# Performance work log

Measured on AMD Instinct MI355X. Metric: run time of the kernel, lower is better.

## Reference

```python
import jax, jax.numpy as jnp
import numpy as np

B, N, C, H, W = 4, 262144, 40, 256, 256
HID = 128


def _bilinear_sample(plane, u, v):
    """torch F.grid_sample(mode='bilinear', padding_mode='zeros', align_corners=False).
    plane: (B, C, H, W); u, v: (B, N) in [-1, 1] (u -> width axis, v -> height axis).
    Returns (B, N, C)."""
    Wd, Hd = plane.shape[3], plane.shape[2]
    ix = ((u + 1.0) * Wd - 1.0) * 0.5
    iy = ((v + 1.0) * Hd - 1.0) * 0.5
    ix0 = jnp.floor(ix)
    iy0 = jnp.floor(iy)
    fx = ix - ix0
    fy = iy - iy0
    ix0 = ix0.astype(jnp.int32)
    iy0 = iy0.astype(jnp.int32)
    flat = plane.reshape(plane.shape[0], plane.shape[1], Hd * Wd)  # (B,C,H*W)

    def corner(xi, yi, w):
        valid = (xi >= 0) & (xi < Wd) & (yi >= 0) & (yi < Hd)
        xc = jnp.clip(xi, 0, Wd - 1)
        yc = jnp.clip(yi, 0, Hd - 1)
        idx = yc * Wd + xc  # (B,N)
        vals = jnp.take_along_axis(flat, idx[:, None, :], axis=2)  # (B,C,N)
        return vals * (w * valid)[:, None, :]

    out = (corner(ix0, iy0, (1 - fx) * (1 - fy))
           + corner(ix0 + 1, iy0, fx * (1 - fy))
           + corner(ix0, iy0 + 1, (1 - fx) * fy)
           + corner(ix0 + 1, iy0 + 1, fx * fy))  # (B,C,N)
    return jnp.transpose(out, (0, 2, 1))  # (B,N,C)


def _sample_triplane(triplane, coords):
    x, y, z = coords[..., 0], coords[..., 1], coords[..., 2]
    f_xy = _bilinear_sample(triplane[:, 0], x, y)
    f_xz = _bilinear_sample(triplane[:, 1], x, z)
    f_yz = _bilinear_sample(triplane[:, 2], y, z)
    return jnp.concatenate([f_xy, f_xz, f_yz], axis=-1)  # (B,N,3C)


def setup_inputs() -> dict:
    key = jax.random.key(0)
    ks = jax.random.split(key, 16)
    triplane = jax.random.normal(ks[0], (B, 3, C, H, W), dtype=jnp.float32)
    coords = jax.random.uniform(ks[1], (B, N, 3), dtype=jnp.float32) * 2.0 - 1.0
    vd = jax.random.normal(ks[2], (B, N, 3), dtype=jnp.float32)
    view_dirs = vd / (jnp.linalg.norm(vd, axis=-1, keepdims=True) + 1e-8)
    s = 0.05
    p = {
        'triplane': triplane, 'coords': coords, 'view_dirs': view_dirs,
        'dw1': jax.random.normal(ks[3], (3 * C, HID), dtype=jnp.float32) * s,
        'db1': jnp.zeros((HID,), jnp.float32),
        'dw2': jax.random.normal(ks[4], (HID, HID), dtype=jnp.float32) * s,
        'db2': jnp.zeros((HID,), jnp.float32),
        'dw3': jax.random.normal(ks[5], (HID, 1), dtype=jnp.float32) * s,
        'db3': jnp.zeros((1,), jnp.float32),
        'cw1': jax.random.normal(ks[6], (3 * C + 3, HID), dtype=jnp.float32) * s,
        'cb1': jnp.zeros((HID,), jnp.float32),
        'cw2': jax.random.normal(ks[7], (HID, HID), dtype=jnp.float32) * s,
        'cb2': jnp.zeros((HID,), jnp.float32),
        'cw3': jax.random.normal(ks[8], (HID, 3), dtype=jnp.float32) * s,
        'cb3': jnp.zeros((3,), jnp.float32),
    }
    return p


def reference(triplane, coords, view_dirs, dw1, db1, dw2, db2, dw3, db3,
              cw1, cb1, cw2, cb2, cw3, cb3):
    feats = _sample_triplane(triplane, coords)  # (B,N,3C)
    h = jax.nn.relu(feats @ dw1 + db1)
    h = jax.nn.relu(h @ dw2 + db2)
    density = h @ dw3 + db3  # (B,N,1)
    cin = jnp.concatenate([feats, view_dirs], axis=-1)
    g = jax.nn.relu(cin @ cw1 + cb1)
    g = jax.nn.relu(g @ cw2 + cb2)
    rgb = jax.nn.sigmoid(g @ cw3 + cb3)  # (B,N,3)
    return density, rgb
```

## Files before the change

### kernel.cpp

```cpp
#include <hip/hip_runtime.h>
#include <cstdint>
#include <cstddef>

typedef __bf16 bf16x8 __attribute__((ext_vector_type(8)));
typedef float  f32x4  __attribute__((ext_vector_type(4)));

#define MFMA16(a,b,c) __builtin_amdgcn_mfma_f32_16x16x32_bf16((a),(b),(c),0,0,0)

__device__ __forceinline__ uint f2bf1(float f){
  uint u = __builtin_bit_cast(uint, f);
  u += 0x7FFFu + ((u >> 16) & 1u);
  return u >> 16;
}
__device__ __forceinline__ uint pack2(float a, float b){
  return f2bf1(a) | (f2bf1(b) << 16);
}
__device__ __forceinline__ uint pack2f(float a, float b){
  uint ua = __builtin_bit_cast(uint, a) + 0x8000u;
  uint ub = __builtin_bit_cast(uint, b) + 0x8000u;
  return __builtin_amdgcn_perm(ub, ua, 0x07060302u);
}
__device__ __forceinline__ float bflo(uint d){ return __builtin_bit_cast(float, d << 16); }
__device__ __forceinline__ float bfhi(uint d){ return __builtin_bit_cast(float, d & 0xFFFF0000u); }

__global__ __launch_bounds__(256, 4) void transpose_k(
    const float* __restrict__ tri, ushort* __restrict__ tp)
{
  __shared__ ushort st[64 * 41];
  const int bi  = blockIdx.x;
  const int xb  = bi & 3;
  const int y   = (bi >> 2) & 255;
  const int q   = bi >> 10;
  const int tid = threadIdx.x;
  const float* src = tri + (size_t)q * 40 * 65536 + y * 256 + xb * 64;
#pragma unroll
  for (int it = 0; it < 10; it++){
    int lin = it * 256 + tid;
    int c = lin >> 6, x = lin & 63;
    float v = src[(size_t)c * 65536 + x];
    st[x * 41 + c] = (ushort)f2bf1(v);
  }
  __syncthreads();
  uint* dst = (uint*)(tp + ((size_t)q * 65536 + (size_t)y * 256 + xb * 64) * 40);
#pragma unroll
  for (int it = 0; it < 5; it++){
    int lin = it * 256 + tid;
    int e  = lin * 2;
    int x1 = (e * 1639) >> 16;       int c1 = e  - x1 * 40;
    int e2 = e + 1;
    int x2 = (e2 * 1639) >> 16;      int c2 = e2 - x2 * 40;
    dst[lin] = (uint)st[x1 * 41 + c1] | ((uint)st[x2 * 41 + c2] << 16);
  }
}

__global__ void pack_k(const float* __restrict__ dw1, const float* __restrict__ cw1,
                       const float* __restrict__ dw2, const float* __restrict__ cw2,
                       const float* __restrict__ dw3, const float* __restrict__ cw3,
                       uint4* __restrict__ wpk)
{
  int idx = blockIdx.x * 256 + threadIdx.x;
  if (idx >= 8704) return;
  int mode, rel;
  if      (idx < 2048){ mode = 0; rel = idx; }
  else if (idx < 4096){ mode = 1; rel = idx - 2048; }
  else if (idx < 6144){ mode = 2; rel = idx - 4096; }
  else if (idx < 8192){ mode = 3; rel = idx - 6144; }
  else if (idx < 8448){ mode = 4; rel = idx - 8192; }
  else                { mode = 5; rel = idx - 8448; }
  int frag = rel >> 6, lane = rel & 63;
  int Mt = frag >> 2, s = frag & 3;
  int m  = Mt * 16 + (lane & 15);
  int kb = s * 32 + (lane >> 4) * 8;
  uint d[4];
#pragma unroll
  for (int jj = 0; jj < 4; jj++){
    float v0 = 0.f, v1 = 0.f;
#pragma unroll
    for (int h = 0; h < 2; h++){
      int k = kb + jj * 2 + h;
      float v = 0.f;
      switch (mode){
        case 0: v = (k < 120) ? dw1[k * 128 + m] : 0.f; break;
        case 1: v = (k < 123) ? cw1[k * 128 + m] : 0.f; break;
        case 2: v = dw2[k * 128 + m]; break;
        case 3: v = cw2[k * 128 + m]; break;
        case 4: v = (m == 0) ? dw3[k] : 0.f; break;
        default: v = (m >= 1 && m <= 3) ? cw3[k * 3 + (m - 1)] : 0.f; break;
      }
      if (h == 0) v0 = v; else v1 = v;
    }
    d[jj] = pack2(v0, v1);
  }
  uint4 o; o.x = d[0]; o.y = d[1]; o.z = d[2]; o.w = d[3];
  wpk[idx] = o;
}

__device__ __forceinline__ uint4 blend4(uint4 a, uint4 b, uint4 c, uint4 d,
                                        float w00, float w10, float w01, float w11){
  uint4 ov;
  ov.x = pack2f(w00*bflo(a.x)+w10*bflo(b.x)+w01*bflo(c.x)+w11*bflo(d.x),
                w00*bfhi(a.x)+w10*bfhi(b.x)+w01*bfhi(c.x)+w11*bfhi(d.x));
  ov.y = pack2f(w00*bflo(a.y)+w10*bflo(b.y)+w01*bflo(c.y)+w11*bflo(d.y),
                w00*bfhi(a.y)+w10*bfhi(b.y)+w01*bfhi(c.y)+w11*bfhi(d.y));
  ov.z = pack2f(w00*bflo(a.z)+w10*bflo(b.z)+w01*bflo(c.z)+w11*bflo(d.z),
                w00*bfhi(a.z)+w10*bfhi(b.z)+w01*bfhi(c.z)+w11*bfhi(d.z));
  ov.w = pack2f(w00*bflo(a.w)+w10*bflo(b.w)+w01*bflo(c.w)+w11*bflo(d.w),
                w00*bfhi(a.w)+w10*bfhi(b.w)+w01*bfhi(c.w)+w11*bfhi(d.w));
  return ov;
}

__device__ __forceinline__ bf16x8 read_h(const uint* S, int s, int t, int lrow, int lq){
  int dwb = (s * 16 + lq * 4 + (lrow << 2)) & 63;
  return __builtin_bit_cast(bf16x8, *(const uint4*)&S[(t * 16 + lrow) * 64 + dwb]);
}

__device__ __forceinline__ void put_h(uint* S, f32x4 v, int Mt, int t, int lrow, int lq){
  uint2 w;
  w.x = pack2f(fmaxf(v[0], 0.f), fmaxf(v[1], 0.f));
  w.y = pack2f(fmaxf(v[2], 0.f), fmaxf(v[3], 0.f));
  int dw = (Mt * 8 + lq * 2 + (lrow << 2)) & 63;
  *(uint2*)&S[(t * 16 + lrow) * 64 + dw] = w;
}

__device__ __forceinline__ void layer1(uint* S, const uint4* __restrict__ W,
                                       const float* __restrict__ bias,
                                       const uint4 (&bf)[4][2],
                                       int lrow, int lq, int lane){
  f32x4 acc[8][2];
#pragma unroll
  for (int Mt = 0; Mt < 8; Mt++){
    f32x4 bi = *(const f32x4*)(bias + Mt * 16 + lq * 4);
    acc[Mt][0] = bi; acc[Mt][1] = bi;
  }
#pragma unroll
  for (int s = 0; s < 4; s++)
#pragma unroll
    for (int Mt = 0; Mt < 8; Mt++){
      bf16x8 aw = __builtin_bit_cast(bf16x8, W[(Mt * 4 + s) * 64 + lane]);
      acc[Mt][0] = MFMA16(aw, __builtin_bit_cast(bf16x8, bf[s][0]), acc[Mt][0]);
      acc[Mt][1] = MFMA16(aw, __builtin_bit_cast(bf16x8, bf[s][1]), acc[Mt][1]);
    }
#pragma unroll
  for (int Mt = 0; Mt < 8; Mt++){
    put_h(S, acc[Mt][0], Mt, 0, lrow, lq);
    put_h(S, acc[Mt][1], Mt, 1, lrow, lq);
  }
}

__device__ __forceinline__ void dense_l(uint* S, const uint4* __restrict__ W,
                                        const float* __restrict__ bias,
                                        int lrow, int lq, int lane){
  f32x4 acc[8][2];
#pragma unroll
  for (int Mt = 0; Mt < 8; Mt++){
    f32x4 bi = *(const f32x4*)(bias + Mt * 16 + lq * 4);
    acc[Mt][0] = bi; acc[Mt][1] = bi;
  }
#pragma unroll
  for (int s = 0; s < 4; s++){
    bf16x8 bh0 = read_h(S, s, 0, lrow, lq);
    bf16x8 bh1 = read_h(S, s, 1, lrow, lq);
#pragma unroll
    for (int Mt = 0; Mt < 8; Mt++){
      bf16x8 aw = __builtin_bit_cast(bf16x8, W[(Mt * 4 + s) * 64 + lane]);
      acc[Mt][0] = MFMA16(aw, bh0, acc[Mt][0]);
      acc[Mt][1] = MFMA16(aw, bh1, acc[Mt][1]);
    }
  }
#pragma unroll
  for (int Mt = 0; Mt < 8; Mt++){
    put_h(S, acc[Mt][0], Mt, 0, lrow, lq);
    put_h(S, acc[Mt][1], Mt, 1, lrow, lq);
  }
}

__device__ __forceinline__ void out_l(const uint* S, const uint4* __restrict__ W,
                                      f32x4 (&acc3)[2], int lrow, int lq, int lane){
#pragma unroll
  for (int s = 0; s < 4; s++){
    bf16x8 aw = __builtin_bit_cast(bf16x8, W[s * 64 + lane]);
    acc3[0] = MFMA16(aw, read_h(S, s, 0, lrow, lq), acc3[0]);
    acc3[1] = MFMA16(aw, read_h(S, s, 1, lrow, lq), acc3[1]);
  }
}

__global__ __launch_bounds__(256, 3) void fused_k(
    const ushort* __restrict__ tp, const float* __restrict__ coords,
    const float* __restrict__ vdirs, const uint4* __restrict__ wpk,
    const float* __restrict__ db1, const float* __restrict__ db2,
    const float* __restrict__ db3, const float* __restrict__ cb1,
    const float* __restrict__ cb2, const float* __restrict__ cb3,
    float* __restrict__ out)
{
  __shared__ uint4 sS4[2048];
  const int wave = threadIdx.x >> 6;
  uint* S = (uint*)sS4 + wave * 2048;
  const int lane = threadIdx.x & 63, lrow = lane & 15, lq = lane >> 4;
  const int blk   = blockIdx.x;
  const int pbase = (blk & 3) * 262144 + (blk >> 2) * 128 + wave * 32;

  uint4 bf[4][2];
#pragma unroll
  for (int t = 0; t < 2; t++){
    const int p  = pbase + t * 16 + lrow;
    const int bb = p >> 18;
    const float cx = coords[3 * p], cy = coords[3 * p + 1], cz = coords[3 * p + 2];
    float pw00[3], pw10[3], pw01[3], pw11[3];
    uint  o00[3], o10[3], o01[3], o11[3];
#pragma unroll
    for (int pl = 0; pl < 3; pl++){
      const float u = (pl == 2) ? cy : cx;
      const float v = (pl == 0) ? cy : cz;
      float ix = fmaf(u, 128.f, 127.5f);
      float iy = fmaf(v, 128.f, 127.5f);
      float fx0 = floorf(ix), fy0 = floorf(iy);
      float fx = ix - fx0, fy = iy - fy0;
      int x0 = (int)fx0, y0 = (int)fy0;
      float wx0 = (x0 >= 0  && x0 < 256) ? (1.f - fx) : 0.f;
      float wx1 = (x0 >= -1 && x0 < 255) ? fx : 0.f;
      float wy0 = (y0 >= 0  && y0 < 256) ? (1.f - fy) : 0.f;
      float wy1 = (y0 >= -1 && y0 < 255) ? fy : 0.f;
      int xc0 = min(max(x0, 0), 255), xc1 = min(max(x0 + 1, 0), 255);
      int yc0 = min(max(y0, 0), 255), yc1 = min(max(y0 + 1, 0), 255);
      pw00[pl] = wx0 * wy0; pw10[pl] = wx1 * wy0;
      pw01[pl] = wx0 * wy1; pw11[pl] = wx1 * wy1;
      o00[pl] = ((uint)yc0 * 256u + (uint)xc0) * 40u;
      o10[pl] = ((uint)yc0 * 256u + (uint)xc1) * 40u;
      o01[pl] = ((uint)yc1 * 256u + (uint)xc0) * 40u;
      o11[pl] = ((uint)yc1 * 256u + (uint)xc1) * 40u;
    }
#pragma unroll
    for (int s = 0; s < 4; s++){
      const int chunk = s * 4 + lq;
      if (chunk == 15){
        const float v0 = vdirs[3 * p], v1 = vdirs[3 * p + 1], v2 = vdirs[3 * p + 2];
        uint4 tt; tt.x = pack2f(v0, v1); tt.y = pack2f(v2, 0.f); tt.z = 0u; tt.w = 0u;
        bf[s][t] = tt;
      } else {
        const int pl = (chunk < 5) ? 0 : (chunk < 10) ? 1 : 2;
        const int c0 = chunk * 8 - pl * 40;
        const ushort* base = tp + (size_t)(bb * 3 + pl) * 2621440 + c0;
        uint4 a = *(const uint4*)(base + o00[pl]);
        uint4 b = *(const uint4*)(base + o10[pl]);
        uint4 c = *(const uint4*)(base + o01[pl]);
        uint4 d = *(const uint4*)(base + o11[pl]);
        bf[s][t] = blend4(a, b, c, d, pw00[pl], pw10[pl], pw01[pl], pw11[pl]);
      }
    }
  }

  f32x4 acc3[2];
  {
    float i0 = (lq == 0) ? db3[0] : 0.f;
    float i1 = (lq == 0) ? cb3[0] : 0.f;
    float i2 = (lq == 0) ? cb3[1] : 0.f;
    float i3 = (lq == 0) ? cb3[2] : 0.f;
    f32x4 iv = {i0, i1, i2, i3};
    acc3[0] = iv; acc3[1] = iv;
  }

  layer1 (S, wpk + 0,    db1, bf, lrow, lq, lane);
  dense_l(S, wpk + 4096, db2,     lrow, lq, lane);
  out_l  (S, wpk + 8192, acc3,    lrow, lq, lane);
  layer1 (S, wpk + 2048, cb1, bf, lrow, lq, lane);
  dense_l(S, wpk + 6144, cb2,     lrow, lq, lane);
  out_l  (S, wpk + 8448, acc3,    lrow, lq, lane);

  if (lq == 0){
#pragma unroll
    for (int t = 0; t < 2; t++){
      int p = pbase + t * 16 + lrow;
      out[p] = acc3[t][0];
      float* rgb = out + 1048576 + (size_t)p * 3;
      rgb[0] = 1.f / (1.f + __expf(-acc3[t][1]));
      rgb[1] = 1.f / (1.f + __expf(-acc3[t][2]));
      rgb[2] = 1.f / (1.f + __expf(-acc3[t][3]));
    }
  }
}

extern "C" void kernel_launch(void* const* d_in, const int* in_sizes, int n_in,
                              void* d_out, int out_size, void* d_ws, size_t ws_size,
                              hipStream_t stream)
{
  (void)in_sizes; (void)n_in; (void)out_size; (void)ws_size;
  const float* tri    = (const float*)d_in[0];
  const float* coords = (const float*)d_in[1];
  const float* vdirs  = (const float*)d_in[2];
  const float* dw1 = (const float*)d_in[3];  const float* db1 = (const float*)d_in[4];
  const float* dw2 = (const float*)d_in[5];  const float* db2 = (const float*)d_in[6];
  const float* dw3 = (const float*)d_in[7];  const float* db3 = (const float*)d_in[8];
  const float* cw1 = (const float*)d_in[9];  const float* cb1 = (const float*)d_in[10];
  const float* cw2 = (const float*)d_in[11]; const float* cb2 = (const float*)d_in[12];
  const float* cw3 = (const float*)d_in[13]; const float* cb3 = (const float*)d_in[14];

  char* ws = (char*)d_ws;
  const size_t planes_bytes = 62914560;
  ushort* tp  = (ushort*)ws;
  uint4*  wpk = (uint4*)(ws + planes_bytes);

  transpose_k<<<12288, 256, 0, stream>>>(tri, tp);
  pack_k<<<34, 256, 0, stream>>>(dw1, cw1, dw2, cw2, dw3, cw3, wpk);
  fused_k<<<8192, 256, 0, stream>>>(tp, coords, vdirs, wpk,
                                    db1, db2, db3, cb1, cb2, cb3,
                                    (float*)d_out);
}
```

Before: 663.5 us.

## Stage MLP weights into LDS with double-buffered async loads, merge prep kernels

The fused kernel now runs 512-thread blocks and stages each layer's packed bf16 weights into double-buffered LDS using global_load_lds. The next layer's weights load while the current layer's MFMAs run. This replaces per-wave global/L2 weight fetches in the inner MFMA loops. The transpose and weight-pack kernels are merged into one launch to save a kernel launch. It uses 128 KB of dynamic LDS per block and adds block-wide barriers between layers, which can lower occupancy and serialize waves. There is also a possible ordering issue: no explicit vmcnt wait is issued before the barrier.

```diff
diff --git a/kernel.cpp b/kernel.cpp
--- a/kernel.cpp
+++ b/kernel.cpp
@@ -23,76 +23,87 @@
 __device__ __forceinline__ float bflo(uint d){ return __builtin_bit_cast(float, d << 16); }
 __device__ __forceinline__ float bfhi(uint d){ return __builtin_bit_cast(float, d & 0xFFFF0000u); }
 
-__global__ __launch_bounds__(256, 4) void transpose_k(
-    const float* __restrict__ tri, ushort* __restrict__ tp)
+__global__ __launch_bounds__(256, 4) void prep_k(
+    const float* __restrict__ tri, ushort* __restrict__ tp,
+    const float* __restrict__ dw1, const float* __restrict__ cw1,
+    const float* __restrict__ dw2, const float* __restrict__ cw2,
+    const float* __restrict__ dw3, const float* __restrict__ cw3,
+    uint4* __restrict__ wpk)
 {
   __shared__ ushort st[64 * 41];
-  const int bi  = blockIdx.x;
-  const int xb  = bi & 3;
-  const int y   = (bi >> 2) & 255;
-  const int q   = bi >> 10;
   const int tid = threadIdx.x;
-  const float* src = tri + (size_t)q * 40 * 65536 + y * 256 + xb * 64;
-#pragma unroll
-  for (int it = 0; it < 10; it++){
-    int lin = it * 256 + tid;
-    int c = lin >> 6, x = lin & 63;
-    float v = src[(size_t)c * 65536 + x];
-    st[x * 41 + c] = (ushort)f2bf1(v);
-  }
-  __syncthreads();
-  uint* dst = (uint*)(tp + ((size_t)q * 65536 + (size_t)y * 256 + xb * 64) * 40);
-#pragma unroll
-  for (int it = 0; it < 5; it++){
-    int lin = it * 256 + tid;
-    int e  = lin * 2;
-    int x1 = (e * 1639) >> 16;       int c1 = e  - x1 * 40;
-    int e2 = e + 1;
-    int x2 = (e2 * 1639) >> 16;      int c2 = e2 - x2 * 40;
-    dst[lin] = (uint)st[x1 * 41 + c1] | ((uint)st[x2 * 41 + c2] << 16);
-  }
-}
-
-__global__ void pack_k(const float* __restrict__ dw1, const float* __restrict__ cw1,
-                       const float* __restrict__ dw2, const float* __restrict__ cw2,
-                       const float* __restrict__ dw3, const float* __restrict__ cw3,
-                       uint4* __restrict__ wpk)
-{
-  int idx = blockIdx.x * 256 + threadIdx.x;
-  if (idx >= 8704) return;
-  int mode, rel;
-  if      (idx < 2048){ mode = 0; rel = idx; }
-  else if (idx < 4096){ mode = 1; rel = idx - 2048; }
-  else if (idx < 6144){ mode = 2; rel = idx - 4096; }
-  else if (idx < 8192){ mode = 3; rel = idx - 6144; }
-  else if (idx < 8448){ mode = 4; rel = idx - 8192; }
-  else                { mode = 5; rel = idx - 8448; }
-  int frag = rel >> 6, lane = rel & 63;
-  int Mt = frag >> 2, s = frag & 3;
-  int m  = Mt * 16 + (lane & 15);
-  int kb = s * 32 + (lane >> 4) * 8;
-  uint d[4];
-#pragma unroll
-  for (int jj = 0; jj < 4; jj++){
-    float v0 = 0.f, v1 = 0.f;
-#pragma unroll
-    for (int h = 0; h < 2; h++){
-      int k = kb + jj * 2 + h;
-      float v = 0.f;
-      switch (mode){
-        case 0: v = (k < 120) ? dw1[k * 128 + m] : 0.f; break;
-        case 1: v = (k < 123) ? cw1[k * 128 + m] : 0.f; break;
-        case 2: v = dw2[k * 128 + m]; break;
-        case 3: v = cw2[k * 128 + m]; break;
-        case 4: v = (m == 0) ? dw3[k] : 0.f; break;
-        default: v = (m >= 1 && m <= 3) ? cw3[k * 3 + (m - 1)] : 0.f; break;
+  if (blockIdx.x < 12288){
+    const int bi  = blockIdx.x;
+    const int xb  = bi & 3;
+    const int y   = (bi >> 2) & 255;
+    const int q   = bi >> 10;
+    const float* src = tri + (size_t)q * 40 * 65536 + y * 256 + xb * 64;
+#pragma unroll
+    for (int it = 0; it < 10; it++){
+      int lin = it * 256 + tid;
+      int c = lin >> 6, x = lin & 63;
+      float v = src[(size_t)c * 65536 + x];
+      st[x * 41 + c] = (ushort)f2bf1(v);
+    }
+    __syncthreads();
+    uint* dst = (uint*)(tp + ((size_t)q * 65536 + (size_t)y * 256 + xb * 64) * 40);
+#pragma unroll
+    for (int it = 0; it < 5; it++){
+      int lin = it * 256 + tid;
+      int e  = lin * 2;
+      int x1 = (e * 1639) >> 16;       int c1 = e  - x1 * 40;
+      int e2 = e + 1;
+      int x2 = (e2 * 1639) >> 16;      int c2 = e2 - x2 * 40;
+      dst[lin] = (uint)st[x1 * 41 + c1] | ((uint)st[x2 * 41 + c2] << 16);
+    }
+  } else {
+    int idx = (blockIdx.x - 12288) * 256 + tid;
+    if (idx >= 8704) return;
+    int mode, rel;
+    if      (idx < 2048){ mode = 0; rel = idx; }
+    else if (idx < 4096){ mode = 1; rel = idx - 2048; }
+    else if (idx < 6144){ mode = 2; rel = idx - 4096; }
+    else if (idx < 8192){ mode = 3; rel = idx - 6144; }
+    else if (idx < 8448){ mode = 4; rel = idx - 8192; }
+    else                { mode = 5; rel = idx - 8448; }
+    int frag = rel >> 6, lane = rel & 63;
+    int Mt = frag >> 2, s = frag & 3;
+    int m  = Mt * 16 + (lane & 15);
+    int kb = s * 32 + (lane >> 4) * 8;
+    uint d[4];
+#pragma unroll
+    for (int jj = 0; jj < 4; jj++){
+      float v0 = 0.f, v1 = 0.f;
+#pragma unroll
+      for (int h = 0; h < 2; h++){
+        int k = kb + jj * 2 + h;
+        float v = 0.f;
+        switch (mode){
+          case 0: v = (k < 120) ? dw1[k * 128 + m] : 0.f; break;
+          case 1: v = (k < 123) ? cw1[k * 128 + m] : 0.f; break;
+          case 2: v = dw2[k * 128 + m]; break;
+          case 3: v = cw2[k * 128 + m]; break;
+          case 4: v = (m == 0) ? dw3[k] : 0.f; break;
+          default: v = (m >= 1 && m <= 3) ? cw3[k * 3 + (m - 1)] : 0.f; break;
+        }
+        if (h == 0) v0 = v; else v1 = v;
       }
-      if (h == 0) v0 = v; else v1 = v;
-    }
-    d[jj] = pack2(v0, v1);
-  }
-  uint4 o; o.x = d[0]; o.y = d[1]; o.z = d[2]; o.w = d[3];
-  wpk[idx] = o;
+      d[jj] = pack2(v0, v1);
+    }
+    uint4 o; o.x = d[0]; o.y = d[1]; o.z = d[2]; o.w = d[3];
+    wpk[idx] = o;
+  }
+}
+
+__device__ __forceinline__ void stage_w(const uint4* __restrict__ g,
+                                        uint4* l, int wave, int lane, int n){
+  const int chunks = n >> 6;
+  for (int c = wave; c < chunks; c += 8){
+    __builtin_amdgcn_global_load_lds(
+      (const __attribute__((address_space(1))) void*)(g + c * 64 + lane),
+      (__attribute__((address_space(3))) void*)(l + c * 64 + lane),
+      16, 0, 0);
+  }
 }
 
 __device__ __forceinline__ uint4 blend4(uint4 a, uint4 b, uint4 c, uint4 d,
@@ -122,7 +133,7 @@
   *(uint2*)&S[(t * 16 + lrow) * 64 + dw] = w;
 }
 
-__device__ __forceinline__ void layer1(uint* S, const uint4* __restrict__ W,
+__device__ __forceinline__ void layer1(uint* S, const uint4* W,
                                        const float* __restrict__ bias,
                                        const uint4 (&bf)[4][2],
                                        int lrow, int lq, int lane){
@@ -147,7 +158,7 @@
   }
 }
 
-__device__ __forceinline__ void dense_l(uint* S, const uint4* __restrict__ W,
+__device__ __forceinline__ void dense_l(uint* S, const uint4* W,
                                         const float* __restrict__ bias,
                                         int lrow, int lq, int lane){
   f32x4 acc[8][2];
@@ -174,7 +185,7 @@
   }
 }
 
-__device__ __forceinline__ void out_l(const uint* S, const uint4* __restrict__ W,
+__device__ __forceinline__ void out_l(const uint* S, const uint4* W,
                                       f32x4 (&acc3)[2], int lrow, int lq, int lane){
 #pragma unroll
   for (int s = 0; s < 4; s++){
@@ -184,7 +195,7 @@
   }
 }
 
-__global__ __launch_bounds__(256, 3) void fused_k(
+__global__ __launch_bounds__(512, 2) void fused_k(
     const ushort* __restrict__ tp, const float* __restrict__ coords,
     const float* __restrict__ vdirs, const uint4* __restrict__ wpk,
     const float* __restrict__ db1, const float* __restrict__ db2,
@@ -192,12 +203,16 @@
     const float* __restrict__ cb2, const float* __restrict__ cb3,
     float* __restrict__ out)
 {
-  __shared__ uint4 sS4[2048];
+  extern __shared__ uint4 smem[];
   const int wave = threadIdx.x >> 6;
-  uint* S = (uint*)sS4 + wave * 2048;
+  uint*  S   = (uint*)(smem + (size_t)wave * 512);
+  uint4* WB0 = smem + 4096;
+  uint4* WB1 = smem + 6144;
   const int lane = threadIdx.x & 63, lrow = lane & 15, lq = lane >> 4;
   const int blk   = blockIdx.x;
-  const int pbase = (blk & 3) * 262144 + (blk >> 2) * 128 + wave * 32;
+  const int pbase = (blk & 3) * 262144 + (blk >> 2) * 256 + wave * 32;
+
+  stage_w(wpk + 0, WB0, wave, lane, 2048);
 
   uint4 bf[4][2];
 #pragma unroll
@@ -259,12 +274,29 @@
     acc3[0] = iv; acc3[1] = iv;
   }
 
-  layer1 (S, wpk + 0,    db1, bf, lrow, lq, lane);
-  dense_l(S, wpk + 4096, db2,     lrow, lq, lane);
-  out_l  (S, wpk + 8192, acc3,    lrow, lq, lane);
-  layer1 (S, wpk + 2048, cb1, bf, lrow, lq, lane);
-  dense_l(S, wpk + 6144, cb2,     lrow, lq, lane);
-  out_l  (S, wpk + 8448, acc3,    lrow, lq, lane);
+  __syncthreads();
+
+  stage_w(wpk + 4096, WB1, wave, lane, 2048);
+  layer1 (S, WB0, db1, bf, lrow, lq, lane);
+  __syncthreads();
+
+  stage_w(wpk + 8192, WB0, wave, lane, 256);
+  dense_l(S, WB1, db2, lrow, lq, lane);
+  __syncthreads();
+
+  stage_w(wpk + 2048, WB1, wave, lane, 2048);
+  out_l  (S, WB0, acc3, lrow, lq, lane);
+  __syncthreads();
+
+  stage_w(wpk + 6144, WB0, wave, lane, 2048);
+  layer1 (S, WB1, cb1, bf, lrow, lq, lane);
+  __syncthreads();
+
+  stage_w(wpk + 8448, WB1, wave, lane, 256);
+  dense_l(S, WB0, cb2, lrow, lq, lane);
+  __syncthreads();
+
+  out_l  (S, WB1, acc3, lrow, lq, lane);
 
   if (lq == 0){
 #pragma unroll
@@ -299,9 +331,11 @@
   ushort* tp  = (ushort*)ws;
   uint4*  wpk = (uint4*)(ws + planes_bytes);
 
-  transpose_k<<<12288, 256, 0, stream>>>(tri, tp);
-  pack_k<<<34, 256, 0, stream>>>(dw1, cw1, dw2, cw2, dw3, cw3, wpk);
-  fused_k<<<8192, 256, 0, stream>>>(tp, coords, vdirs, wpk,
-                                    db1, db2, db3, cb1, cb2, cb3,
-                                    (float*)d_out);
-}
+  (void)hipFuncSetAttribute((const void*)fused_k,
+                            hipFuncAttributeMaxDynamicSharedMemorySize, 131072);
+
+  prep_k<<<12322, 256, 0, stream>>>(tri, tp, dw1, cw1, dw2, cw2, dw3, cw3, wpk);
+  fused_k<<<4096, 512, 131072, stream>>>(tp, coords, vdirs, wpk,
+                                         db1, db2, db3, cb1, cb2, cb3,
+                                         (float*)d_out);
+}
```

Result: faster. 643.7 us (-3.0%).
